# Kernel optimization log

Hardware: AMD Instinct MI355X
Metric: run time of the kernel (lower is better)

## Reference

```python
import jax, jax.numpy as jnp
import numpy as np

D = 1024

def setup_inputs() -> dict:
    key = jax.random.key(0)
    ks = jax.random.split(key, 7)
    s = 1.0 / np.sqrt(D)
    x = jax.random.normal(ks[0], (4, 4096, D), dtype=jnp.float32)
    Wi = jax.random.uniform(ks[1], (2 * D, D), jnp.float32, -s, s)   # in_proj weight [2D, D]
    bi = jax.random.uniform(ks[2], (2 * D,), jnp.float32, -s, s)
    Wc = jax.random.uniform(ks[3], (D, 1, 3), jnp.float32, -0.577, 0.577)  # depthwise conv [D,1,3]
    bc = jax.random.uniform(ks[4], (D,), jnp.float32, -0.577, 0.577)
    Wo = jax.random.uniform(ks[5], (D, D), jnp.float32, -s, s)       # out_proj weight [D, D]
    bo = jax.random.uniform(ks[6], (D,), jnp.float32, -s, s)
    return {"x": x, "Wi": Wi, "bi": bi, "Wc": Wc, "bc": bc, "Wo": Wo, "bo": bo}

def _depthwise_conv1d(v, Wc, bc):
    # v: [B, L, D] -> NCH [B, D, L]; kernel [D, 1, 3] (OIH), groups = D; pad 1 both sides
    y = jax.lax.conv_general_dilated(
        v.transpose(0, 2, 1), Wc,
        window_strides=(1,), padding=[(1, 1)],
        dimension_numbers=("NCH", "OIH", "NCH"),
        feature_group_count=v.shape[-1])
    return y.transpose(0, 2, 1) + bc  # [B, L, D]

def reference(x, Wi, bi, Wc, bc, Wo, bo):
    uv = jnp.einsum("bld,ed->ble", x, Wi) + bi        # [B, L, 2D]
    u, v = jnp.split(uv, 2, axis=-1)                   # each [B, L, D]
    y = _depthwise_conv1d(v, Wc, bc)
    y = jax.nn.silu(y) * u                             # fused gate
    return jnp.einsum("bld,ed->ble", y, Wo) + bo       # [B, L, D]
```

## Files before the change

kernel.cpp:

```cpp
#include <hip/hip_runtime.h>
#include <math.h>


typedef __attribute__((ext_vector_type(8))) short short8;
typedef __attribute__((ext_vector_type(4))) float floatx4;

__device__ __forceinline__ float b2f(short s) {
    unsigned int u = ((unsigned int)(unsigned short)s) << 16;
    float f;
    __builtin_memcpy(&f, &u, 4);
    return f;
}

__device__ __forceinline__ short f2b(float f) {
    unsigned int u;
    __builtin_memcpy(&u, &f, 4);
    u += 0x7fffu + ((u >> 16) & 1u);
    return (short)(u >> 16);
}

__device__ __forceinline__ void gl_lds16(const short* g, short* l) {
    __builtin_amdgcn_global_load_lds(
        (const __attribute__((address_space(1))) unsigned int*)g,
        (__attribute__((address_space(3))) unsigned int*)l,
        16, 0, 0);
}

__global__ __launch_bounds__(256) void cvt_all(
    const float* __restrict__ x, const float* __restrict__ Wi,
    const float* __restrict__ Wo, short* __restrict__ xb,
    short* __restrict__ Wib, short* __restrict__ Wob)
{
    constexpr int n1 = 16384 * 1024 / 8;
    constexpr int n2 = 2048 * 1024 / 8;
    constexpr int n3 = 1024 * 1024 / 8;
    int i = blockIdx.x * 256 + threadIdx.x;
    const float* src;
    short* dst;
    int j;
    if (i < n1)           { src = x;  dst = xb;  j = i; }
    else if (i < n1 + n2) { src = Wi; dst = Wib; j = i - n1; }
    else if (i < n1 + n2 + n3) { src = Wo; dst = Wob; j = i - n1 - n2; }
    else return;
    float4 a = ((const float4*)src)[2 * j];
    float4 b = ((const float4*)src)[2 * j + 1];
    short8 o;
    o[0] = f2b(a.x); o[1] = f2b(a.y); o[2] = f2b(a.z); o[3] = f2b(a.w);
    o[4] = f2b(b.x); o[5] = f2b(b.y); o[6] = f2b(b.z); o[7] = f2b(b.w);
    ((short8*)dst)[j] = o;
}

template <bool OUTF32>
__global__ __launch_bounds__(256, 3) void gemm_bt(
    const short* __restrict__ A, const short* __restrict__ B,
    const float* __restrict__ bias, void* __restrict__ Cv,
    int lda, int ldb, int ldc)
{
    constexpr int K = 1024;
    __shared__ __attribute__((aligned(16))) short As[128 * 64];
    __shared__ __attribute__((aligned(16))) short Bs[128 * 64];

    const int tid  = threadIdx.x;
    const int wave = tid >> 6;
    const int lane = tid & 63;
    const int mBase = blockIdx.y * 128;
    const int nBase = blockIdx.x * 128;

    floatx4 acc[4][4];
#pragma unroll
    for (int i = 0; i < 4; i++)
#pragma unroll
        for (int j = 0; j < 4; j++) acc[i][j] = {0.f, 0.f, 0.f, 0.f};

    const int sRow = wave * 32 + (lane >> 3);
    const int sg   = (((lane & 7) ^ ((lane >> 3) & 7))) * 8;
    const short* gA = A + (size_t)(mBase + sRow) * lda + sg;
    const short* gB = B + (size_t)(nBase + sRow) * ldb + sg;
    short* lA = &As[(wave * 32) * 64];
    short* lB = &Bs[(wave * 32) * 64];

    const int mq = (wave & 1) * 64;
    const int nq = (wave >> 1) * 64;
    const int fRow = lane & 15;
    const int lg   = lane >> 4;
    const int p0   = ((lg ^ (fRow & 7))) * 8;

    for (int k0 = 0; k0 < K; k0 += 64) {
        __syncthreads();
#pragma unroll
        for (int j = 0; j < 4; j++) {
            gl_lds16(gA + (size_t)(8 * j) * lda + k0, lA + 8 * j * 64);
            gl_lds16(gB + (size_t)(8 * j) * ldb + k0, lB + 8 * j * 64);
        }
        __syncthreads();

#pragma unroll
        for (int h = 0; h < 2; h++) {
            const int po = p0 ^ (h * 32);
            short8 a[4], b[4];
#pragma unroll
            for (int mi = 0; mi < 4; mi++)
                a[mi] = *(const short8*)&As[(mq + mi * 16 + fRow) * 64 + po];
#pragma unroll
            for (int ni = 0; ni < 4; ni++)
                b[ni] = *(const short8*)&Bs[(nq + ni * 16 + fRow) * 64 + po];
#pragma unroll
            for (int mi = 0; mi < 4; mi++)
#pragma unroll
                for (int ni = 0; ni < 4; ni++)
                    acc[mi][ni] = __builtin_amdgcn_mfma_f32_16x16x32_bf16(
                        a[mi], b[ni], acc[mi][ni], 0, 0, 0);
        }
    }

    const int colq = lane & 15;
    const int rowq = (lane >> 4) * 4;
#pragma unroll
    for (int ni = 0; ni < 4; ni++) {
        const int col = nBase + nq + ni * 16 + colq;
        const float bv = bias[col];
#pragma unroll
        for (int mi = 0; mi < 4; mi++) {
            const int row = mBase + mq + mi * 16 + rowq;
#pragma unroll
            for (int r = 0; r < 4; r++) {
                float v = acc[mi][ni][r] + bv;
                if (OUTF32)
                    ((float*)Cv)[(size_t)(row + r) * ldc + col] = v;
                else
                    ((short*)Cv)[(size_t)(row + r) * ldc + col] = f2b(v);
            }
        }
    }
}

__global__ __launch_bounds__(256) void conv_gate(
    const short* __restrict__ uv, const float* __restrict__ Wc,
    const float* __restrict__ bc, short* __restrict__ yb)
{
    const int idx = blockIdx.x * 256 + threadIdx.x;
    const int d8 = idx & 127;
    const int m  = idx >> 7;
    const int l  = m & 4095;
    const int d  = d8 * 8;

    float w[24];
#pragma unroll
    for (int q = 0; q < 6; q++)
        *(float4*)&w[q * 4] = ((const float4*)(Wc + d * 3))[q];
    float bcv[8];
    *(float4*)&bcv[0] = ((const float4*)(bc + d))[0];
    *(float4*)&bcv[4] = ((const float4*)(bc + d))[1];

    const size_t rowu = (size_t)m * 2048 + d;
    const size_t rowv = rowu + 1024;

    const short8 z = {0, 0, 0, 0, 0, 0, 0, 0};
    const short8 us = *(const short8*)(uv + rowu);
    const short8 vc = *(const short8*)(uv + rowv);
    const short8 vm = (l > 0)    ? *(const short8*)(uv + rowv - 2048) : z;
    const short8 vp = (l < 4095) ? *(const short8*)(uv + rowv + 2048) : z;

    short8 outv;
#pragma unroll
    for (int j = 0; j < 8; j++) {
        float y = b2f(vm[j]) * w[j * 3 + 0]
                + b2f(vc[j]) * w[j * 3 + 1]
                + b2f(vp[j]) * w[j * 3 + 2]
                + bcv[j];
        float sil = y / (1.0f + expf(-y));
        outv[j] = f2b(sil * b2f(us[j]));
    }
    *(short8*)(yb + (size_t)m * 1024 + d) = outv;
}

extern "C" void kernel_launch(void* const* d_in, const int* in_sizes, int n_in,
                              void* d_out, int out_size, void* d_ws, size_t ws_size,
                              hipStream_t stream)
{
    const float* x  = (const float*)d_in[0];
    const float* Wi = (const float*)d_in[1];
    const float* bi = (const float*)d_in[2];
    const float* Wc = (const float*)d_in[3];
    const float* bc = (const float*)d_in[4];
    const float* Wo = (const float*)d_in[5];
    const float* bo = (const float*)d_in[6];
    float* out = (float*)d_out;

    short* wsS = (short*)d_ws;
    short* uv  = wsS;
    short* xb  = uv + (size_t)16384 * 2048;
    short* Wib = xb + (size_t)16384 * 1024;
    short* Wob = Wib + (size_t)2048 * 1024;

    dim3 blk(256);

    constexpr int nCvt = (16384 * 1024 + 2048 * 1024 + 1024 * 1024) / 8;
    cvt_all<<<(nCvt + 255) / 256, blk, 0, stream>>>(x, Wi, Wo, xb, Wib, Wob);

    dim3 g1(2048 / 128, 16384 / 128);
    gemm_bt<false><<<g1, blk, 0, stream>>>(xb, Wib, bi, uv, 1024, 1024, 2048);

    conv_gate<<<(16384 * 128) / 256, blk, 0, stream>>>(uv, Wc, bc, xb);

    dim3 g2(1024 / 128, 16384 / 128);
    gemm_bt<true><<<g2, blk, 0, stream>>>(xb, Wob, bo, out, 1024, 1024, 1024);
}
```

Measured before the change: 283.9 us.

## Pipeline GEMM with 4-stage LDS ring and larger 256x256 tiles

The GEMM kernel moves to 512-thread blocks computing 256x256 output tiles with a K step of 32. A 4-slot shared-memory ring is prefetched three stages ahead via global_load_lds, gated by vmcnt waits and barriers, so global loads overlap MFMA work. It also raises wave priority around the MFMA loop. The aim is to cut per-iteration load stalls and raise operand reuse, at the cost of 128 KB of LDS per block, more accumulator registers and fewer resident blocks per CU.

```diff
diff --git a/kernel.cpp b/kernel.cpp
--- a/kernel.cpp
+++ b/kernel.cpp
@@ -51,80 +51,113 @@
 }
 
 template <bool OUTF32>
-__global__ __launch_bounds__(256, 3) void gemm_bt(
+__global__ __launch_bounds__(512, 2) void gemm_bt(
     const short* __restrict__ A, const short* __restrict__ B,
     const float* __restrict__ bias, void* __restrict__ Cv,
     int lda, int ldb, int ldc)
 {
-    constexpr int K = 1024;
-    __shared__ __attribute__((aligned(16))) short As[128 * 64];
-    __shared__ __attribute__((aligned(16))) short Bs[128 * 64];
+    constexpr int K  = 1024;
+    constexpr int NT = K / 32;
+    __shared__ __attribute__((aligned(16))) short As[4 * 8192];
+    __shared__ __attribute__((aligned(16))) short Bs[4 * 8192];
 
     const int tid  = threadIdx.x;
     const int wave = tid >> 6;
     const int lane = tid & 63;
-    const int mBase = blockIdx.y * 128;
-    const int nBase = blockIdx.x * 128;
-
-    floatx4 acc[4][4];
-#pragma unroll
-    for (int i = 0; i < 4; i++)
+    const int mBase = blockIdx.y * 256;
+    const int nBase = blockIdx.x * 256;
+
+    floatx4 acc[8][4];
+#pragma unroll
+    for (int i = 0; i < 8; i++)
 #pragma unroll
         for (int j = 0; j < 4; j++) acc[i][j] = {0.f, 0.f, 0.f, 0.f};
 
-    const int sRow = wave * 32 + (lane >> 3);
-    const int sg   = (((lane & 7) ^ ((lane >> 3) & 7))) * 8;
-    const short* gA = A + (size_t)(mBase + sRow) * lda + sg;
-    const short* gB = B + (size_t)(nBase + sRow) * ldb + sg;
-    short* lA = &As[(wave * 32) * 64];
-    short* lB = &Bs[(wave * 32) * 64];
-
-    const int mq = (wave & 1) * 64;
-    const int nq = (wave >> 1) * 64;
+    const int srow = lane >> 2;
+    const int sg   = ((lane & 3) ^ ((srow >> 1) & 3)) * 8;
+    const short* gA = A + (size_t)(mBase + wave * 32 + srow) * lda + sg;
+    const short* gB = B + (size_t)(nBase + wave * 32 + srow) * ldb + sg;
+    short* lA0 = &As[wave * 1024];
+    short* lB0 = &Bs[wave * 1024];
+
+    auto stage = [&](int kk, int slot) {
+#pragma unroll
+        for (int j = 0; j < 2; j++) {
+            gl_lds16(gA + (size_t)(16 * j) * lda + kk, lA0 + slot * 8192 + j * 512);
+            gl_lds16(gB + (size_t)(16 * j) * ldb + kk, lB0 + slot * 8192 + j * 512);
+        }
+    };
+
     const int fRow = lane & 15;
     const int lg   = lane >> 4;
-    const int p0   = ((lg ^ (fRow & 7))) * 8;
-
-    for (int k0 = 0; k0 < K; k0 += 64) {
-        __syncthreads();
-#pragma unroll
-        for (int j = 0; j < 4; j++) {
-            gl_lds16(gA + (size_t)(8 * j) * lda + k0, lA + 8 * j * 64);
-            gl_lds16(gB + (size_t)(8 * j) * ldb + k0, lB + 8 * j * 64);
-        }
-        __syncthreads();
-
-#pragma unroll
-        for (int h = 0; h < 2; h++) {
-            const int po = p0 ^ (h * 32);
-            short8 a[4], b[4];
-#pragma unroll
-            for (int mi = 0; mi < 4; mi++)
-                a[mi] = *(const short8*)&As[(mq + mi * 16 + fRow) * 64 + po];
+    const int pg8  = (lg ^ ((fRow >> 1) & 3)) * 8;
+    const int mq   = (wave >> 2) * 128;
+    const int nq   = (wave & 3) * 64;
+    const int aBase = (mq + fRow) * 32 + pg8;
+    const int bBase = (nq + fRow) * 32 + pg8;
+
+    auto compute = [&](int slot) {
+        const short* Ab = &As[slot * 8192];
+        const short* Bb = &Bs[slot * 8192];
+        short8 av[8], bv[4];
+#pragma unroll
+        for (int mi = 0; mi < 8; mi++)
+            av[mi] = *(const short8*)&Ab[aBase + mi * 512];
+#pragma unroll
+        for (int ni = 0; ni < 4; ni++)
+            bv[ni] = *(const short8*)&Bb[bBase + ni * 512];
+        __builtin_amdgcn_s_setprio(1);
+#pragma unroll
+        for (int mi = 0; mi < 8; mi++)
 #pragma unroll
             for (int ni = 0; ni < 4; ni++)
-                b[ni] = *(const short8*)&Bs[(nq + ni * 16 + fRow) * 64 + po];
-#pragma unroll
-            for (int mi = 0; mi < 4; mi++)
-#pragma unroll
-                for (int ni = 0; ni < 4; ni++)
-                    acc[mi][ni] = __builtin_amdgcn_mfma_f32_16x16x32_bf16(
-                        a[mi], b[ni], acc[mi][ni], 0, 0, 0);
-        }
+                acc[mi][ni] = __builtin_amdgcn_mfma_f32_16x16x32_bf16(
+                    av[mi], bv[ni], acc[mi][ni], 0, 0, 0);
+        __builtin_amdgcn_s_setprio(0);
+    };
+
+    stage(0, 0);
+    stage(32, 1);
+    stage(64, 2);
+
+    for (int t = 0; t < NT - 3; ++t) {
+        stage((t + 3) * 32, (t + 3) & 3);
+        asm volatile("s_waitcnt vmcnt(12)" ::: "memory");
+        __builtin_amdgcn_s_barrier();
+        asm volatile("" ::: "memory");
+        compute(t & 3);
+        asm volatile("" ::: "memory");
+        __builtin_amdgcn_s_barrier();
+        asm volatile("" ::: "memory");
     }
 
+    asm volatile("s_waitcnt vmcnt(8)" ::: "memory");
+    __builtin_amdgcn_s_barrier();
+    asm volatile("" ::: "memory");
+    compute((NT - 3) & 3);
+    __builtin_amdgcn_s_barrier();
+    asm volatile("s_waitcnt vmcnt(4)" ::: "memory");
+    __builtin_amdgcn_s_barrier();
+    asm volatile("" ::: "memory");
+    compute((NT - 2) & 3);
+    __builtin_amdgcn_s_barrier();
+    asm volatile("s_waitcnt vmcnt(0)" ::: "memory");
+    __builtin_amdgcn_s_barrier();
+    asm volatile("" ::: "memory");
+    compute((NT - 1) & 3);
+
     const int colq = lane & 15;
-    const int rowq = (lane >> 4) * 4;
+    const int rowq = lg * 4;
 #pragma unroll
     for (int ni = 0; ni < 4; ni++) {
         const int col = nBase + nq + ni * 16 + colq;
-        const float bv = bias[col];
-#pragma unroll
-        for (int mi = 0; mi < 4; mi++) {
+        const float bvv = bias[col];
+#pragma unroll
+        for (int mi = 0; mi < 8; mi++) {
             const int row = mBase + mq + mi * 16 + rowq;
 #pragma unroll
             for (int r = 0; r < 4; r++) {
-                float v = acc[mi][ni][r] + bv;
+                float v = acc[mi][ni][r] + bvv;
                 if (OUTF32)
                     ((float*)Cv)[(size_t)(row + r) * ldc + col] = v;
                 else
@@ -194,15 +227,16 @@
     short* Wob = Wib + (size_t)2048 * 1024;
 
     dim3 blk(256);
+    dim3 blkG(512);
 
     constexpr int nCvt = (16384 * 1024 + 2048 * 1024 + 1024 * 1024) / 8;
     cvt_all<<<(nCvt + 255) / 256, blk, 0, stream>>>(x, Wi, Wo, xb, Wib, Wob);
 
-    dim3 g1(2048 / 128, 16384 / 128);
-    gemm_bt<false><<<g1, blk, 0, stream>>>(xb, Wib, bi, uv, 1024, 1024, 2048);
+    dim3 g1(2048 / 256, 16384 / 256);
+    gemm_bt<false><<<g1, blkG, 0, stream>>>(xb, Wib, bi, uv, 1024, 1024, 2048);
 
     conv_gate<<<(16384 * 128) / 256, blk, 0, stream>>>(uv, Wc, bc, xb);
 
-    dim3 g2(1024 / 128, 16384 / 128);
-    gemm_bt<true><<<g2, blk, 0, stream>>>(xb, Wob, bo, out, 1024, 1024, 1024);
-}
+    dim3 g2(1024 / 256, 16384 / 256);
+    gemm_bt<true><<<g2, blkG, 0, stream>>>(xb, Wob, bo, out, 1024, 1024, 1024);
+}
```

Result: slower. 310.9 us (+9.5%).
